# Kernel tuning notes

Measured on AMD Instinct MI355X. Metric: run time of the kernel, lower is better.

## Reference

```python
import jax, jax.numpy as jnp
import numpy as np

N = 100000      # points
K = 16          # neighbors (nsample)
C_IN = 128      # d_in
C_OUT = 256     # d_out
NK = 15         # kernel points (k_015)
SIGMA = 0.3
SCALE = SIGMA ** 2 * 2 + 1e-10
BN_EPS = 1e-5


def setup_inputs() -> dict:
    key = jax.random.key(0)
    ks = jax.random.split(key, 6)
    p = jax.random.normal(ks[0], (N, 3), dtype=jnp.float32)
    x = jax.random.normal(ks[1], (N, C_IN), dtype=jnp.float32)
    idx = jax.random.randint(ks[2], (N, K), 0, N, dtype=jnp.int32)
    kernel_point = jax.random.normal(ks[3], (1, NK, 3), dtype=jnp.float32) * 0.5
    conv_w = jax.random.normal(ks[4], (C_OUT, C_IN + 3, NK), dtype=jnp.float32) * 0.02
    conv_b = jax.random.normal(ks[5], (C_OUT,), dtype=jnp.float32) * 0.02
    bn_gamma = jnp.ones((C_OUT,), dtype=jnp.float32)
    bn_beta = jnp.zeros((C_OUT,), dtype=jnp.float32)
    bn_mean = jnp.zeros((C_OUT,), dtype=jnp.float32)
    bn_var = jnp.ones((C_OUT,), dtype=jnp.float32)
    return {"p": p, "x": x, "kernel_point": kernel_point, "conv_w": conv_w,
            "conv_b": conv_b, "bn_gamma": bn_gamma, "bn_beta": bn_beta,
            "bn_mean": bn_mean, "bn_var": bn_var, "idx": idx}


def reference(p, x, kernel_point, conv_w, conv_b, bn_gamma, bn_beta, bn_mean, bn_var, idx):
    # --- queryandgroup (use_xyz=True), neighbor indices precomputed ---
    pj = p[idx] - p[:, None, :]        # [N, K, 3] relative coords
    xj = x[idx]                        # [N, K, C_IN]
    # --- DepthwiseKPConv (first_layer branch: d_in != d_out) ---
    l2 = jnp.linalg.norm(pj, axis=2, keepdims=True)               # [N, K, 1]
    pj = pj / (jnp.max(l2, axis=1, keepdims=True) + 1e-10)        # normalize by max neighbor dist
    diff = kernel_point[:, :, None, :] - pj[:, None, :, :]        # [N, NK, K, 3]
    corr = jnp.exp(-jnp.sum(diff * diff, axis=-1) / SCALE)        # [N, NK, K]
    xj = jnp.concatenate([pj, xj], axis=-1)                       # [N, K, C_IN+3]
    agg = jnp.einsum('nmk,nkc->nmc', corr, xj)                    # [N, NK, C_IN+3]
    # Conv1d(C_IN+3, C_OUT, kernel=NK): full contraction over channel & kernel axes
    y = jnp.einsum('nmc,ocm->no', agg, conv_w) + conv_b           # [N, C_OUT]
    # BatchNorm1d (eval stats) + ReLU
    y = (y - bn_mean) * (bn_gamma / jnp.sqrt(bn_var + BN_EPS)) + bn_beta
    return jax.nn.relu(y)
```

## Files before the change

kernel.cpp:

```cpp
#include <hip/hip_runtime.h>
#include <hip/hip_fp16.h>

#define N_PTS   100000
#define KNB     16
#define CIN     128
#define COUT    256
#define NKP     15
#define CCH     131
#define MSTR    136
#define KP      2048
#define MPAD    100096
#define CHROWS  25600

typedef _Float16 f16x8 __attribute__((ext_vector_type(8)));
typedef float    f32x4 __attribute__((ext_vector_type(4)));
typedef int      i32x4 __attribute__((ext_vector_type(4)));

__device__ __forceinline__ void g2lds16(const void* g, void* l) {
  __builtin_amdgcn_global_load_lds((const __attribute__((address_space(1))) void*)g,
                                   (__attribute__((address_space(3))) void*)l, 16, 0, 0);
}

__global__ __launch_bounds__(256) void k_prep_w(
    const float* __restrict__ w, const float* __restrict__ cb,
    const float* __restrict__ g, const float* __restrict__ be,
    const float* __restrict__ mu, const float* __restrict__ var,
    __half* __restrict__ wt, float* __restrict__ sc, float* __restrict__ sh) {
  int gid = blockIdx.x * 256 + threadIdx.x;
  int o = gid / KP, r = gid - o * KP;
  float v = 0.f;
  if (r < NKP * MSTR) {
    int m = r / MSTR, c = r - m * MSTR;
    if (c < 128)      v = w[(o * CCH + (c + 3)) * NKP + m];
    else if (c < 131) v = w[(o * CCH + (c - 128)) * NKP + m];
  }
  wt[gid] = __float2half(v);
  if (gid < COUT) {
    float s = g[gid] / sqrtf(var[gid] + 1e-5f);
    sc[gid] = s;
    sh[gid] = (cb[gid] - mu[gid]) * s + be[gid];
  }
}

#define XROW 140
__global__ __launch_bounds__(256) void k_agg(
    const float* __restrict__ p, const float* __restrict__ x,
    const float* __restrict__ kp, const int* __restrict__ idx,
    __half* __restrict__ agg, int r0) {
  __shared__ _Float16 xj[4][33 * XROW];
  __shared__ float pj[4][16][4];
  __shared__ float co[4][16][16];
  const int l = threadIdx.x & 63;
  const int w = threadIdx.x >> 6;
  const int n = r0 + blockIdx.x * 4 + w;
  const int nc = (n < N_PTS) ? n : (N_PTS - 1);
  const int nbr = idx[nc * KNB + (l & 15)];

  {
    _Float16* xz = &xj[w][0];
    #pragma unroll
    for (int j = 0; j < 18; j++)
      *(f16x8*)(xz + (l + 64 * j) * 8 * 0 + 0) , (void)0;
  }
  {
    char* xz = (char*)&xj[w][0];
    long2 z2 = {0, 0};
    #pragma unroll
    for (int j = 0; j < 18; j++)
      *(long*)(xz + 8 * (l + 64 * j)) = 0;
  }

  const float cx = p[nc * 3], cy = p[nc * 3 + 1], cz = p[nc * 3 + 2];
  float ax = p[nbr * 3]     - cx;
  float ay = p[nbr * 3 + 1] - cy;
  float az = p[nbr * 3 + 2] - cz;
  float mx = sqrtf(ax * ax + ay * ay + az * az);
  #pragma unroll
  for (int d = 1; d < 16; d <<= 1) mx = fmaxf(mx, __shfl_xor(mx, d));
  const float inv = 1.0f / (mx + 1e-10f);
  ax *= inv; ay *= inv; az *= inv;

  #define LQ(K) (*(const float2*)(x + (size_t)(unsigned)__builtin_amdgcn_readlane(nbr, (K)) * CIN + 2 * l))
  float2 q[16];
  #pragma unroll
  for (int k = 0; k < 16; k++) q[k] = LQ(k);

  if (l < 16) {
    pj[w][l][0] = ax; pj[w][l][1] = ay; pj[w][l][2] = az; pj[w][l][3] = 0.f;
    xj[w][l * XROW + 128] = (_Float16)ax;
    xj[w][l * XROW + 129] = (_Float16)ay;
    xj[w][l * XROW + 130] = (_Float16)az;
  }
  __syncthreads();

  const int k1 = l >> 2;
  f32x4 pv = *(const f32x4*)&pj[w][k1][0];
  f32x4 cc;
  #pragma unroll
  for (int j = 0; j < 4; j++) {
    int m = (l & 3) * 4 + j;
    if (m < 15) {
      float dx = kp[m * 3] - pv[0], dy = kp[m * 3 + 1] - pv[1], dz = kp[m * 3 + 2] - pv[2];
      cc[j] = __expf((dx * dx + dy * dy + dz * dz) * -5.5555553f);
    } else cc[j] = 0.f;
  }
  *(f32x4*)&co[w][k1][(l & 3) * 4] = cc;

  #pragma unroll
  for (int k = 0; k < 16; k++) {
    __half2 h = __floats2half2_rn(q[k].x, q[k].y);
    *(__half2*)&xj[w][k * XROW + 2 * l] = h;
  }
  __syncthreads();

  f16x8 af = {};
  if (l < 32) {
    #pragma unroll
    for (int i = 0; i < 8; i++)
      af[i] = (_Float16)co[w][(l >> 4) * 8 + i][l & 15];
  }

  const bool live = (n < N_PTS);
  __half* ar = agg + (size_t)(n - r0) * KP;
  const int cfix = l & 15;
  const int g4 = (l >> 4) * 4;

  #pragma unroll
  for (int c0 = 0; c0 <= 128; c0 += 16) {
    f16x8 bf = {};
    if (l < 32) {
      const _Float16* xb = &xj[w][(l >> 4) * 8 * XROW + c0 + cfix];
      #pragma unroll
      for (int i = 0; i < 8; i++) bf[i] = xb[i * XROW];
    }
    f32x4 d = __builtin_amdgcn_mfma_f32_16x16x32_f16(af, bf, (f32x4){0.f, 0.f, 0.f, 0.f}, 0, 0, 0);
    if (live) {
      const int c = c0 + cfix;
      #pragma unroll
      for (int i = 0; i < 4; i++) {
        const int m = g4 + i;
        if (m < 15 && c < 136)
          ar[m * MSTR + c] = __float2half(d[i]);
      }
    }
  }
  if (live && l == 0) {
    i32x4 z = {0, 0, 0, 0};
    *(i32x4*)((char*)ar + 4080) = z;
  }
}

__global__ __launch_bounds__(256) void k_gemm(
    const __half* __restrict__ A, const __half* __restrict__ B,
    const float* __restrict__ sc, const float* __restrict__ sh,
    float* __restrict__ out, int r0) {
  __shared__ __align__(16) __half Al[128 * 64];
  __shared__ __align__(16) __half Bl[128 * 64];
  const int t = threadIdx.x;
  const int l = t & 63;
  const int bn = blockIdx.x, bm = blockIdx.y;
  const int m0 = bm * 128, n0 = bn * 128;
  const int w = t >> 6;
  const int wm = w >> 1, wn = w & 1;

  f32x4 acc[4][4] = {};

  const int arow = t >> 3;
  const int kb   = (t & 7) << 4;
  const int kbsw = kb ^ ((arow & 7) << 4);
  const char* aSrc = (const char*)(A + (size_t)(m0 + arow) * KP) + kbsw;
  const char* bSrc = (const char*)(B + (size_t)(n0 + arow) * KP) + kbsw;
  char* aDst = (char*)Al + t * 16;
  char* bDst = (char*)Bl + t * 16;
  const size_t rowStride32 = (size_t)32 * KP * 2;

  for (int kt = 0; kt < KP / 64; kt++) {
    __syncthreads();
    #pragma unroll
    for (int i = 0; i < 4; i++) {
      g2lds16(aSrc + i * rowStride32 + (size_t)kt * 128, aDst + i * 4096);
      g2lds16(bSrc + i * rowStride32 + (size_t)kt * 128, bDst + i * 4096);
    }
    __syncthreads();
    #pragma unroll
    for (int kk = 0; kk < 2; kk++) {
      f16x8 af[4], bf[4];
      const int rbyte = ((l >> 4) << 4) + kk * 64;
      #pragma unroll
      for (int i = 0; i < 4; i++) {
        const int ra = wm * 64 + i * 16 + (l & 15);
        af[i] = *(const f16x8*)((const char*)Al + ra * 128 + (rbyte ^ ((ra & 7) << 4)));
        const int rb = wn * 64 + i * 16 + (l & 15);
        bf[i] = *(const f16x8*)((const char*)Bl + rb * 128 + (rbyte ^ ((rb & 7) << 4)));
      }
      #pragma unroll
      for (int i = 0; i < 4; i++)
        #pragma unroll
        for (int j = 0; j < 4; j++)
          acc[i][j] = __builtin_amdgcn_mfma_f32_16x16x32_f16(af[i], bf[j], acc[i][j], 0, 0, 0);
    }
  }

  #pragma unroll
  for (int j = 0; j < 4; j++) {
    const int col = n0 + wn * 64 + j * 16 + (l & 15);
    const float s = sc[col], h = sh[col];
    #pragma unroll
    for (int i = 0; i < 4; i++) {
      const int rr = r0 + m0 + wm * 64 + i * 16 + ((l >> 4) << 2);
      #pragma unroll
      for (int rg = 0; rg < 4; rg++) {
        const int r = rr + rg;
        if (r < N_PTS) {
          float v = acc[i][j][rg] * s + h;
          out[(size_t)r * COUT + col] = fmaxf(v, 0.f);
        }
      }
    }
  }
}

extern "C" void kernel_launch(void* const* d_in, const int* in_sizes, int n_in,
                              void* d_out, int out_size, void* d_ws, size_t ws_size,
                              hipStream_t stream) {
  (void)in_sizes; (void)n_in; (void)out_size;
  const float* p   = (const float*)d_in[0];
  const float* x   = (const float*)d_in[1];
  const float* kp  = (const float*)d_in[2];
  const float* w   = (const float*)d_in[3];
  const float* cb  = (const float*)d_in[4];
  const float* g   = (const float*)d_in[5];
  const float* be  = (const float*)d_in[6];
  const float* mu  = (const float*)d_in[7];
  const float* var = (const float*)d_in[8];
  const int* idx   = (const int*)d_in[9];
  float* out = (float*)d_out;

  char* ws = (char*)d_ws;
  size_t off = 0;
  __half* wt  = (__half*)(ws + off); off += (size_t)COUT * KP * 2;
  float*  sc  = (float*)(ws + off);  off += 1024;
  float*  sh  = (float*)(ws + off);  off += 1024;
  __half* agg = (__half*)(ws + off);
  size_t avail = (ws_size > off) ? (ws_size - off) : 0;

  size_t maxrows = avail / ((size_t)KP * 2);
  int rows = CHROWS;
  if (maxrows < (size_t)rows) rows = (int)(maxrows & ~(size_t)127);
  if (rows < 128) rows = 128;

  hipLaunchKernelGGL(k_prep_w, dim3(COUT * KP / 256), dim3(256), 0, stream,
                     w, cb, g, be, mu, var, wt, sc, sh);

  for (int row0 = 0; row0 < N_PTS; row0 += rows) {
    int rr = MPAD - row0;
    if (rr > rows) rr = rows;
    hipLaunchKernelGGL(k_agg, dim3(rr / 4), dim3(256), 0, stream, p, x, kp, idx, agg, row0);
    hipLaunchKernelGGL(k_gemm, dim3(2, rr / 128), dim3(256), 0, stream, agg, wt, sc, sh, out, row0);
  }
}
```

Measured before the change: 565.1 us.

## Gather neighbor features directly into MFMA operands and store aggregation channel-major

The aggregation kernel no longer stages gathered neighbor features through shared memory. Each lane now reads fp32 features straight from global memory into MFMA operand registers. The intermediate buffer changes from kernel-point-major rows to a channel-major layout with the 16 kernel points innermost. That allows contiguous 8-byte vector stores and drops the scattered scalar half stores and padding writes. The weight prep is reordered to match, and K grows from 2048 to 2112, so the GEMM does slightly more work and the buffer gets slightly larger. The global gathers are also less coalesced than the old wide row loads.

```diff
diff --git a/kernel.cpp b/kernel.cpp
--- a/kernel.cpp
+++ b/kernel.cpp
@@ -7,14 +7,13 @@
 #define COUT    256
 #define NKP     15
 #define CCH     131
-#define MSTR    136
-#define KP      2048
+#define KP      2112
 #define MPAD    100096
-#define CHROWS  25600
+#define CHROWS  25088
 
 typedef _Float16 f16x8 __attribute__((ext_vector_type(8)));
 typedef float    f32x4 __attribute__((ext_vector_type(4)));
-typedef int      i32x4 __attribute__((ext_vector_type(4)));
+typedef unsigned int u32x2 __attribute__((ext_vector_type(2)));
 
 __device__ __forceinline__ void g2lds16(const void* g, void* l) {
   __builtin_amdgcn_global_load_lds((const __attribute__((address_space(1))) void*)g,
@@ -28,11 +27,11 @@
     __half* __restrict__ wt, float* __restrict__ sc, float* __restrict__ sh) {
   int gid = blockIdx.x * 256 + threadIdx.x;
   int o = gid / KP, r = gid - o * KP;
+  int c = r >> 4, m = r & 15;
   float v = 0.f;
-  if (r < NKP * MSTR) {
-    int m = r / MSTR, c = r - m * MSTR;
-    if (c < 128)      v = w[(o * CCH + (c + 3)) * NKP + m];
-    else if (c < 131) v = w[(o * CCH + (c - 128)) * NKP + m];
+  if (m < 15 && c < 131) {
+    int refch = (c < 128) ? (c + 3) : (c - 128);
+    v = w[(o * CCH + refch) * NKP + m];
   }
   wt[gid] = __float2half(v);
   if (gid < COUT) {
@@ -42,12 +41,10 @@
   }
 }
 
-#define XROW 140
 __global__ __launch_bounds__(256) void k_agg(
     const float* __restrict__ p, const float* __restrict__ x,
     const float* __restrict__ kp, const int* __restrict__ idx,
     __half* __restrict__ agg, int r0) {
-  __shared__ _Float16 xj[4][33 * XROW];
   __shared__ float pj[4][16][4];
   __shared__ float co[4][16][16];
   const int l = threadIdx.x & 63;
@@ -56,20 +53,6 @@
   const int nc = (n < N_PTS) ? n : (N_PTS - 1);
   const int nbr = idx[nc * KNB + (l & 15)];
 
-  {
-    _Float16* xz = &xj[w][0];
-    #pragma unroll
-    for (int j = 0; j < 18; j++)
-      *(f16x8*)(xz + (l + 64 * j) * 8 * 0 + 0) , (void)0;
-  }
-  {
-    char* xz = (char*)&xj[w][0];
-    long2 z2 = {0, 0};
-    #pragma unroll
-    for (int j = 0; j < 18; j++)
-      *(long*)(xz + 8 * (l + 64 * j)) = 0;
-  }
-
   const float cx = p[nc * 3], cy = p[nc * 3 + 1], cz = p[nc * 3 + 2];
   float ax = p[nbr * 3]     - cx;
   float ay = p[nbr * 3 + 1] - cy;
@@ -80,17 +63,12 @@
   const float inv = 1.0f / (mx + 1e-10f);
   ax *= inv; ay *= inv; az *= inv;
 
-  #define LQ(K) (*(const float2*)(x + (size_t)(unsigned)__builtin_amdgcn_readlane(nbr, (K)) * CIN + 2 * l))
-  float2 q[16];
-  #pragma unroll
-  for (int k = 0; k < 16; k++) q[k] = LQ(k);
-
-  if (l < 16) {
-    pj[w][l][0] = ax; pj[w][l][1] = ay; pj[w][l][2] = az; pj[w][l][3] = 0.f;
-    xj[w][l * XROW + 128] = (_Float16)ax;
-    xj[w][l * XROW + 129] = (_Float16)ay;
-    xj[w][l * XROW + 130] = (_Float16)az;
-  }
+  int rowoff[8];
+  #pragma unroll
+  for (int i = 0; i < 8; i++)
+    rowoff[i] = __shfl(nbr, ((l >> 4) & 1) * 8 + i) * (CIN * 4);
+
+  if (l < 16) { pj[w][l][0] = ax; pj[w][l][1] = ay; pj[w][l][2] = az; pj[w][l][3] = 0.f; }
   __syncthreads();
 
   const int k1 = l >> 2;
@@ -105,12 +83,6 @@
     } else cc[j] = 0.f;
   }
   *(f32x4*)&co[w][k1][(l & 3) * 4] = cc;
-
-  #pragma unroll
-  for (int k = 0; k < 16; k++) {
-    __half2 h = __floats2half2_rn(q[k].x, q[k].y);
-    *(__half2*)&xj[w][k * XROW + 2 * l] = h;
-  }
   __syncthreads();
 
   f16x8 af = {};
@@ -120,33 +92,43 @@
       af[i] = (_Float16)co[w][(l >> 4) * 8 + i][l & 15];
   }
 
+  const bool act  = (l < 32);
   const bool live = (n < N_PTS);
-  __half* ar = agg + (size_t)(n - r0) * KP;
   const int cfix = l & 15;
   const int g4 = (l >> 4) * 4;
-
-  #pragma unroll
-  for (int c0 = 0; c0 <= 128; c0 += 16) {
+  char* outp = (char*)(agg + (size_t)(n - r0) * KP) + cfix * 32 + g4 * 2;
+  const char* xb = (const char*)x + cfix * 4;
+
+  #pragma unroll
+  for (int g = 0; g < 8; g++) {
     f16x8 bf = {};
-    if (l < 32) {
-      const _Float16* xb = &xj[w][(l >> 4) * 8 * XROW + c0 + cfix];
-      #pragma unroll
-      for (int i = 0; i < 8; i++) bf[i] = xb[i * XROW];
+    if (act) {
+      #pragma unroll
+      for (int i = 0; i < 8; i++)
+        bf[i] = (_Float16)(*(const float*)(xb + (size_t)(unsigned)rowoff[i] + g * 64));
     }
     f32x4 d = __builtin_amdgcn_mfma_f32_16x16x32_f16(af, bf, (f32x4){0.f, 0.f, 0.f, 0.f}, 0, 0, 0);
     if (live) {
-      const int c = c0 + cfix;
-      #pragma unroll
-      for (int i = 0; i < 4; i++) {
-        const int m = g4 + i;
-        if (m < 15 && c < 136)
-          ar[m * MSTR + c] = __float2half(d[i]);
-      }
-    }
-  }
-  if (live && l == 0) {
-    i32x4 z = {0, 0, 0, 0};
-    *(i32x4*)((char*)ar + 4080) = z;
+      __half2 h0 = __floats2half2_rn(d[0], d[1]);
+      __half2 h1 = __floats2half2_rn(d[2], d[3]);
+      u32x2 u; u.x = *(unsigned int*)&h0; u.y = *(unsigned int*)&h1;
+      *(u32x2*)(outp + g * 512) = u;
+    }
+  }
+  {
+    f16x8 bf = {};
+    if (act && cfix < 3) {
+      #pragma unroll
+      for (int i = 0; i < 8; i++)
+        bf[i] = (_Float16)pj[w][(l >> 4) * 8 + i][cfix];
+    }
+    f32x4 d = __builtin_amdgcn_mfma_f32_16x16x32_f16(af, bf, (f32x4){0.f, 0.f, 0.f, 0.f}, 0, 0, 0);
+    if (live && cfix < 4) {
+      __half2 h0 = __floats2half2_rn(d[0], d[1]);
+      __half2 h1 = __floats2half2_rn(d[2], d[3]);
+      u32x2 u; u.x = *(unsigned int*)&h0; u.y = *(unsigned int*)&h1;
+      *(u32x2*)(outp + 8 * 512) = u;
+    }
   }
 }
 
```

Result: no change. 570.2 us (+0.9%).
